# Kernel tuning notes

Measured on AMD Instinct MI355X. Metric: run time of the kernel, lower is better.

## Reference

```python
import jax, jax.numpy as jnp
import numpy as np

H = 12      # num attention heads
W = 128     # one-sided window size (band = 2W+1), also the chunk size
G = 32      # number of global tokens (positions 0..G-1)
NEG = -1e9


def setup_inputs() -> dict:
    key = jax.random.key(0)
    ks = jax.random.split(key, 9)
    B, S, D = 1, 4096, 768
    std = 0.02
    f32 = jnp.float32
    return {
        "hidden_states": jax.random.normal(ks[0], (B, S, D), f32),
        "Wq": jax.random.normal(ks[1], (D, D), f32) * std,
        "bq": jnp.zeros((D,), f32),
        "Wk": jax.random.normal(ks[2], (D, D), f32) * std,
        "bk": jnp.zeros((D,), f32),
        "Wv": jax.random.normal(ks[3], (D, D), f32) * std,
        "bv": jnp.zeros((D,), f32),
        "Wo": jax.random.normal(ks[4], (D, D), f32) * std,
        "bo": jnp.zeros((D,), f32),
    }


def _longformer_attn(hidden, Wq, bq, Wk, bk, Wv, bv, Wo, bo):
    B, S, D = hidden.shape
    dh = D // H
    scale = jnp.asarray(dh, hidden.dtype) ** -0.5

    def proj(Wm, bm):
        return (hidden @ Wm + bm).reshape(B, S, H, dh).transpose(0, 2, 1, 3)  # [B,H,S,dh]

    q = proj(Wq, bq) * scale
    k = proj(Wk, bk)
    v = proj(Wv, bv)

    nc = S // W  # number of query chunks
    q_ch = q.reshape(B, H, nc, W, dh)

    # pad keys/values by one chunk on each side; chunk c sees keys [c*W - W, c*W + 2W)
    kp = jnp.pad(k, ((0, 0), (0, 0), (W, W), (0, 0)))
    vp = jnp.pad(v, ((0, 0), (0, 0), (W, W), (0, 0)))
    idx = (jnp.arange(nc) * W)[:, None] + jnp.arange(3 * W)[None, :]  # [nc, 3W] into padded seq
    k_ch = kp[:, :, idx]  # [B,H,nc,3W,dh]
    v_ch = vp[:, :, idx]

    # banded scores via chunked matmul: [B,H,nc,W,3W]
    band = jnp.einsum('bhcqd,bhckd->bhcqk', q_ch, k_ch)

    # exact band mask |i-j| <= W: with local query qi and local key kj (global j = c*W + kj - W)
    qi = jnp.arange(W)[:, None]           # [W,1]
    kj = jnp.arange(3 * W)[None, :]       # [1,3W]
    in_band = (kj >= qi) & (kj <= qi + 2 * W)                     # [W,3W]
    j = (jnp.arange(nc) * W)[:, None, None] + kj[None] - W        # [nc,1,3W] global key index
    valid = in_band[None] & (j >= G) & (j < S)                    # [nc,W,3W]; j<G handled via global path
    band = jnp.where(valid[None, None], band, NEG)
    band = band.reshape(B, H, S, 3 * W)

    # every query also attends to the G global keys
    gsc = jnp.einsum('bhsd,bhgd->bhsg', q, k[:, :, :G])           # [B,H,S,G]
    scores = jnp.concatenate([gsc, band], axis=-1)                # [B,H,S,G+3W]
    probs = jax.nn.softmax(scores, axis=-1)

    out = jnp.einsum('bhsg,bhgd->bhsd', probs[..., :G], v[:, :, :G])
    pb = probs[..., G:].reshape(B, H, nc, W, 3 * W)
    out = out + jnp.einsum('bhcqk,bhckd->bhcqd', pb, v_ch).reshape(B, H, S, dh)

    # global queries attend to everything (full attention on G rows)
    gq_probs = jax.nn.softmax(jnp.einsum('bhgd,bhsd->bhgs', q[:, :, :G], k), axis=-1)
    out_g = jnp.einsum('bhgs,bhsd->bhgd', gq_probs, v)
    out = out.at[:, :, :G].set(out_g)

    out = out.transpose(0, 2, 1, 3).reshape(B, S, D)
    return out @ Wo + bo


def reference(hidden_states, Wq, bq, Wk, bk, Wv, bv, Wo, bo):
    return _longformer_attn(hidden_states, Wq, bq, Wk, bk, Wv, bv, Wo, bo)
```

## Files before the change

kernel.cpp:

```cpp
#include <hip/hip_runtime.h>
#include <stdint.h>

#define S_LEN 4096
#define DMOD  768
#define NH    12
#define DH    64
#define GG    32
#define NEGBIG (-1e9f)

typedef _Float16 f16;
typedef f16 f16x8 __attribute__((ext_vector_type(8)));
typedef f16 f16x4 __attribute__((ext_vector_type(4)));
typedef float f32x4 __attribute__((ext_vector_type(4)));
typedef uint32_t u32;

#define OFF_H16   ((size_t)0)
#define OFF_WT    ((size_t)6291456)
#define OFF_Q     ((size_t)11010048)
#define OFF_K     ((size_t)17301504)
#define OFF_VT    ((size_t)29884416)
#define OFF_ATT   ((size_t)36175872)
#define OFF_GQO   ((size_t)42467328)
#define OFF_GQL   ((size_t)44040192)

__device__ __forceinline__ void gld_lds16(const void* g, void* l) {
  typedef __attribute__((address_space(3))) u32 lds_u32;
  typedef __attribute__((address_space(1))) u32 glb_u32;
  __builtin_amdgcn_global_load_lds((glb_u32*)(uintptr_t)g,
                                   (lds_u32*)(u32)(uintptr_t)l, 16, 0, 0);
}

__global__ __launch_bounds__(256) void prep_kernel(
    const float* __restrict__ hs,
    const float* __restrict__ Wq, const float* __restrict__ Wk,
    const float* __restrict__ Wv, const float* __restrict__ Wo,
    f16* __restrict__ h16, f16* __restrict__ wt)
{
  const int b = blockIdx.x;
  const int t = threadIdx.x;
  if (b < 576) {
    __shared__ float tile[64][65];
    const int w = b / 144, r2 = b % 144;
    const int n0 = (r2 % 12) * 64, k0 = (r2 / 12) * 64;
    const float* W = (w==0) ? Wq : (w==1) ? Wk : (w==2) ? Wv : Wo;
    f16* WT = wt + (size_t)w * DMOD * DMOD;
    #pragma unroll
    for (int rnd = 0; rnd < 4; ++rnd) {
      const int lin = rnd * 1024 + t * 4;
      const int r = lin >> 6, c = lin & 63;
      const float4 vv = *(const float4*)(W + (size_t)(k0 + r) * DMOD + n0 + c);
      tile[r][c+0] = vv.x; tile[r][c+1] = vv.y; tile[r][c+2] = vv.z; tile[r][c+3] = vv.w;
    }
    __syncthreads();
    #pragma unroll
    for (int rnd = 0; rnd < 2; ++rnd) {
      const int lin = rnd * 256 + t;
      const int n = lin >> 3, kc = (lin & 7) * 8;
      f16x8 o;
      #pragma unroll
      for (int j = 0; j < 8; ++j) o[j] = (f16)tile[kc + j][n];
      *(f16x8*)(WT + (size_t)(n0 + n) * DMOD + k0 + kc) = o;
    }
  } else {
    const size_t idx = (size_t)(b - 576) * 2048 + (size_t)t * 8;
    const float4 a = *(const float4*)(hs + idx);
    const float4 c = *(const float4*)(hs + idx + 4);
    f16x8 o;
    o[0]=(f16)a.x; o[1]=(f16)a.y; o[2]=(f16)a.z; o[3]=(f16)a.w;
    o[4]=(f16)c.x; o[5]=(f16)c.y; o[6]=(f16)c.z; o[7]=(f16)c.w;
    *(f16x8*)(h16 + idx) = o;
  }
}

__global__ __launch_bounds__(256) void gemm_qkv(
    const f16* __restrict__ A, const f16* __restrict__ wt,
    const float* __restrict__ bq, const float* __restrict__ bk, const float* __restrict__ bv,
    f16* __restrict__ q16, f16* __restrict__ k16, f16* __restrict__ vt16)
{
  __shared__ __align__(16) f16 At[3][4096];
  __shared__ __align__(16) f16 Bt[3][4096];
  const int z = blockIdx.z;
  const f16* Wt = wt + (size_t)z * DMOD * DMOD;
  const float* bias = (z==0) ? bq : (z==1) ? bk : bv;
  const float scale = (z==0) ? 0.125f : 1.0f;

  const int tid = threadIdx.x;
  const int lane = tid & 63, wid = tid >> 6;
  const int quad = lane >> 4, l15 = lane & 15;
  const int n0 = blockIdx.x * 128, m0 = blockIdx.y * 128;
  const int wm = (wid >> 1) * 64, wn = (wid & 1) * 64;

  f32x4 acc[4][4];
  #pragma unroll
  for (int i=0;i<4;++i)
    #pragma unroll
    for (int j=0;j<4;++j) acc[i][j] = (f32x4){0.f,0.f,0.f,0.f};

  const int lin0 = tid, lin1 = tid + 256;
  const int ar0 = ((lin0>>6)<<4) + (lin0&15), ac0 = ((lin0>>4)&3)*8;
  const int ar1 = ((lin1>>6)<<4) + (lin1&15), ac1 = ((lin1>>4)&3)*8;
  const f16* Ab = A  + (size_t)m0 * DMOD;
  const f16* Bb = Wt + (size_t)n0 * DMOD;

  gld_lds16(Ab + (size_t)ar0*DMOD + ac0, &At[0][lin0*8]);
  gld_lds16(Ab + (size_t)ar1*DMOD + ac1, &At[0][lin1*8]);
  gld_lds16(Bb + (size_t)ar0*DMOD + ac0, &Bt[0][lin0*8]);
  gld_lds16(Bb + (size_t)ar1*DMOD + ac1, &Bt[0][lin1*8]);

  int cur = 0;
  #pragma unroll 3
  for (int k = 0; k < 24; ++k) {
    const int nxt = (cur == 2) ? 0 : cur + 1;
    if (k < 23) {
      const int k0 = (k + 1) * 32;
      gld_lds16(Ab + (size_t)ar0*DMOD + k0 + ac0, &At[nxt][lin0*8]);
      gld_lds16(Ab + (size_t)ar1*DMOD + k0 + ac1, &At[nxt][lin1*8]);
      gld_lds16(Bb + (size_t)ar0*DMOD + k0 + ac0, &Bt[nxt][lin0*8]);
      gld_lds16(Bb + (size_t)ar1*DMOD + k0 + ac1, &Bt[nxt][lin1*8]);
      asm volatile("s_waitcnt vmcnt(4) lgkmcnt(0)" ::: "memory");
    } else {
      asm volatile("s_waitcnt vmcnt(0) lgkmcnt(0)" ::: "memory");
    }
    __builtin_amdgcn_s_barrier();
    f16x8 af[4], bf[4];
    #pragma unroll
    for (int i=0;i<4;++i) {
      af[i] = *(const f16x8*)(&At[cur][((wm>>4)+i)*512 + lane*8]);
      bf[i] = *(const f16x8*)(&Bt[cur][((wn>>4)+i)*512 + lane*8]);
    }
    #pragma unroll
    for (int i=0;i<4;++i)
      #pragma unroll
      for (int j=0;j<4;++j)
        acc[i][j] = __builtin_amdgcn_mfma_f32_16x16x32_f16(af[i], bf[j], acc[i][j], 0, 0, 0);
    cur = nxt;
  }

  if (z < 2) {
    f16* outp = (z==0) ? q16 : k16;
    #pragma unroll
    for (int j=0;j<4;++j) {
      const int col = n0 + wn + j*16 + l15;
      const float bcol = bias[col];
      const int h = col >> 6, d = col & 63;
      #pragma unroll
      for (int i=0;i<4;++i) {
        const int rbase = m0 + wm + i*16 + quad*4;
        f16* dst = outp + ((size_t)h * S_LEN + rbase) * DH + d;
        #pragma unroll
        for (int r=0;r<4;++r)
          dst[(size_t)r * DH] = (f16)((acc[i][j][r] + bcol) * scale);
      }
    }
  } else {
    #pragma unroll
    for (int j=0;j<4;++j) {
      const int col = n0 + wn + j*16 + l15;
      const float bcol = bias[col];
      const int h = col >> 6, d = col & 63;
      #pragma unroll
      for (int i=0;i<4;++i) {
        const int rbase = m0 + wm + i*16 + quad*4;
        f16x4 o;
        #pragma unroll
        for (int r=0;r<4;++r) o[r] = (f16)(acc[i][j][r] + bcol);
        *(f16x4*)(vt16 + ((size_t)h * DH + d) * S_LEN + rbase) = o;
      }
    }
  }
}

__global__ __launch_bounds__(256) void gemm_out(
    const f16* __restrict__ A, const f16* __restrict__ Wt,
    const float* __restrict__ bo, float* __restrict__ outp)
{
  __shared__ __align__(16) f16 At[3][4096];
  __shared__ __align__(16) f16 Bt[3][2048];
  const int tid = threadIdx.x;
  const int lane = tid & 63, wid = tid >> 6;
  const int quad = lane >> 4, l15 = lane & 15;
  const int n0 = blockIdx.x * 64, m0 = blockIdx.y * 128;
  const int wm = (wid >> 1) * 64, wn = (wid & 1) * 32;

  f32x4 acc[4][2];
  #pragma unroll
  for (int i=0;i<4;++i)
    #pragma unroll
    for (int j=0;j<2;++j) acc[i][j] = (f32x4){0.f,0.f,0.f,0.f};

  const int lin0 = tid, lin1 = tid + 256;
  const int ar0 = ((lin0>>6)<<4) + (lin0&15), ac0 = ((lin0>>4)&3)*8;
  const int ar1 = ((lin1>>6)<<4) + (lin1&15), ac1 = ((lin1>>4)&3)*8;
  const f16* Ab = A  + (size_t)m0 * DMOD;
  const f16* Bb = Wt + (size_t)n0 * DMOD;

  gld_lds16(Ab + (size_t)ar0*DMOD + ac0, &At[0][lin0*8]);
  gld_lds16(Ab + (size_t)ar1*DMOD + ac1, &At[0][lin1*8]);
  gld_lds16(Bb + (size_t)ar0*DMOD + ac0, &Bt[0][lin0*8]);

  int cur = 0;
  #pragma unroll 3
  for (int k = 0; k < 24; ++k) {
    const int nxt = (cur == 2) ? 0 : cur + 1;
    if (k < 23) {
      const int k0 = (k + 1) * 32;
      gld_lds16(Ab + (size_t)ar0*DMOD + k0 + ac0, &At[nxt][lin0*8]);
      gld_lds16(Ab + (size_t)ar1*DMOD + k0 + ac1, &At[nxt][lin1*8]);
      gld_lds16(Bb + (size_t)ar0*DMOD + k0 + ac0, &Bt[nxt][lin0*8]);
      asm volatile("s_waitcnt vmcnt(3) lgkmcnt(0)" ::: "memory");
    } else {
      asm volatile("s_waitcnt vmcnt(0) lgkmcnt(0)" ::: "memory");
    }
    __builtin_amdgcn_s_barrier();
    f16x8 af[4], bf[2];
    #pragma unroll
    for (int i=0;i<4;++i)
      af[i] = *(const f16x8*)(&At[cur][((wm>>4)+i)*512 + lane*8]);
    #pragma unroll
    for (int j=0;j<2;++j)
      bf[j] = *(const f16x8*)(&Bt[cur][((wn>>4)+j)*512 + lane*8]);
    #pragma unroll
    for (int i=0;i<4;++i)
      #pragma unroll
      for (int j=0;j<2;++j)
        acc[i][j] = __builtin_amdgcn_mfma_f32_16x16x32_f16(af[i], bf[j], acc[i][j], 0, 0, 0);
    cur = nxt;
  }

  #pragma unroll
  for (int j=0;j<2;++j) {
    const int col = n0 + wn + j*16 + l15;
    const float bcol = bo[col];
    #pragma unroll
    for (int i=0;i<4;++i) {
      const int rbase = m0 + wm + i*16 + quad*4;
      #pragma unroll
      for (int r=0;r<4;++r)
        outp[(size_t)(rbase + r) * DMOD + col] = acc[i][j][r] + bcol;
    }
  }
}

__global__ __launch_bounds__(256) void band_attn(
    const f16* __restrict__ q16, const f16* __restrict__ k16,
    const f16* __restrict__ vt16, f16* __restrict__ att16,
    float* __restrict__ o_part, float* __restrict__ l_part)
{
  __shared__ __align__(16) f16 Pbuf[4][1280];
  const int h = blockIdx.y;
  const int tid = threadIdx.x, lane = tid & 63, wid = tid >> 6;
  const int quad = lane >> 4, l15 = lane & 15;
  f16* P = &Pbuf[wid][0];

  const int bx = blockIdx.x;
  const bool is_gq = (bx >= 32);
  int gr0 = 0, sp = 0, tcount;
  if (is_gq) {
    sp = (bx - 32) * 4 + wid;
    tcount = 8;
  } else {
    const int sub = bx * 4 + wid;
    if (sub == 0) return;
    gr0 = sub * 32;
    tcount = 10;
  }

  const f16* qh = q16 + (size_t)h * S_LEN * DH;
  const f16* kh = k16 + (size_t)h * S_LEN * DH;
  const f16* vh = vt16 + (size_t)h * DH * S_LEN;

  f16x8 aq[2][2];
  #pragma unroll
  for (int mt=0;mt<2;++mt)
    #pragma unroll
    for (int ks=0;ks<2;++ks)
      aq[mt][ks] = *(const f16x8*)(qh + (size_t)(gr0 + mt*16 + l15)*DH + ks*32 + quad*8);

  f32x4 accO[2][4];
  float lacc[2][4];
  #pragma unroll
  for (int mt=0;mt<2;++mt) {
    #pragma unroll
    for (int n=0;n<4;++n) accO[mt][n] = (f32x4){0.f,0.f,0.f,0.f};
    #pragma unroll
    for (int r=0;r<4;++r) lacc[mt][r] = 0.f;
  }

  for (int t = 0; t < tcount; ++t) {
    int j0;
    if (is_gq) {
      j0 = sp*256 + t*32;
    } else if (t > 0) {
      j0 = gr0 - 128 + (t-1)*32;
      if (j0 <= 0 || j0 >= S_LEN) continue;
    } else {
      j0 = 0;
    }
    f16x8 bk[2][2];
    #pragma unroll
    for (int nt=0;nt<2;++nt) {
      const int key = j0 + nt*16 + l15;
      #pragma unroll
      for (int ks=0;ks<2;++ks)
        bk[nt][ks] = *(const f16x8*)(kh + (size_t)key*DH + ks*32 + quad*8);
    }
    f32x4 sc[2][2];
    #pragma unroll
    for (int mt=0;mt<2;++mt)
      #pragma unroll
      for (int nt=0;nt<2;++nt) {
        f32x4 s = __builtin_amdgcn_mfma_f32_16x16x32_f16(aq[mt][0], bk[nt][0],
                                                         (f32x4){0.f,0.f,0.f,0.f}, 0,0,0);
        sc[mt][nt] = __builtin_amdgcn_mfma_f32_16x16x32_f16(aq[mt][1], bk[nt][1], s, 0,0,0);
      }
    if (!is_gq && (t == 1 || t == 9)) {
      #pragma unroll
      for (int nt=0;nt<2;++nt)
        #pragma unroll
        for (int mt=0;mt<2;++mt)
          #pragma unroll
          for (int r=0;r<4;++r) {
            const int e = (nt*16 + l15) - (mt*16 + quad*4 + r);
            const bool ok = (t == 1) ? (e >= 0) : (e <= 0);
            if (!ok) sc[mt][nt][r] = NEGBIG;
          }
    }
    #pragma unroll
    for (int mt=0;mt<2;++mt)
      #pragma unroll
      for (int r=0;r<4;++r) {
        sc[mt][0][r] = __expf(sc[mt][0][r]);
        sc[mt][1][r] = __expf(sc[mt][1][r]);
        lacc[mt][r] += sc[mt][0][r] + sc[mt][1][r];
      }
    #pragma unroll
    for (int mt=0;mt<2;++mt)
      #pragma unroll
      for (int nt=0;nt<2;++nt)
        #pragma unroll
        for (int r=0;r<4;++r)
          P[(mt*16 + quad*4 + r)*40 + nt*16 + l15] = (f16)sc[mt][nt][r];
    asm volatile("s_waitcnt lgkmcnt(0)" ::: "memory");
    f16x8 ap[2];
    #pragma unroll
    for (int mt=0;mt<2;++mt)
      ap[mt] = *(const f16x8*)(P + (mt*16 + l15)*40 + quad*8);
    #pragma unroll
    for (int n=0;n<4;++n) {
      const f16x8 bv = *(const f16x8*)(vh + (size_t)(n*16 + l15)*S_LEN + j0 + quad*8);
      #pragma unroll
      for (int mt=0;mt<2;++mt)
        accO[mt][n] = __builtin_amdgcn_mfma_f32_16x16x32_f16(ap[mt], bv, accO[mt][n], 0,0,0);
    }
  }

  #pragma unroll
  for (int mt=0;mt<2;++mt)
    #pragma unroll
    for (int r=0;r<4;++r) {
      float v = lacc[mt][r];
      v += __shfl_xor(v, 1, 64);
      v += __shfl_xor(v, 2, 64);
      v += __shfl_xor(v, 4, 64);
      v += __shfl_xor(v, 8, 64);
      lacc[mt][r] = v;
    }

  if (is_gq) {
    const int base = (h*16 + sp)*32;
    #pragma unroll
    for (int mt=0;mt<2;++mt)
      #pragma unroll
      for (int r=0;r<4;++r) {
        const int row = mt*16 + quad*4 + r;
        if (l15 == 0) l_part[base+row] = lacc[mt][r];
        #pragma unroll
        for (int n=0;n<4;++n)
          o_part[(size_t)(base+row)*DH + n*16 + l15] = accO[mt][n][r];
      }
  } else {
    #pragma unroll
    for (int mt=0;mt<2;++mt)
      #pragma unroll
      for (int r=0;r<4;++r) {
        const float inv = 1.f / lacc[mt][r];
        const int s = gr0 + mt*16 + quad*4 + r;
        #pragma unroll
        for (int n=0;n<4;++n)
          att16[(size_t)s * DMOD + h*DH + n*16 + l15] = (f16)(accO[mt][n][r] * inv);
      }
  }
}

__global__ __launch_bounds__(256) void gq_merge(
    const float* __restrict__ o_part, const float* __restrict__ l_part,
    f16* __restrict__ att16)
{
  const int h = blockIdx.x;
  const int t = threadIdx.x;
  for (int u = t; u < 512; u += 256) {
    const int row = u >> 4, c4 = u & 15;
    float4 s = {0.f,0.f,0.f,0.f};
    float l = 0.f;
    for (int sp=0;sp<16;++sp) {
      const int base = (h*16 + sp)*32 + row;
      const float4 v = *(const float4*)&o_part[(size_t)base*DH + c4*4];
      s.x += v.x; s.y += v.y; s.z += v.z; s.w += v.w;
      l += l_part[base];
    }
    const float inv = 1.f / l;
    f16x4 o;
    o[0] = (f16)(s.x*inv); o[1] = (f16)(s.y*inv);
    o[2] = (f16)(s.z*inv); o[3] = (f16)(s.w*inv);
    *(f16x4*)&att16[(size_t)row * DMOD + h*DH + c4*4] = o;
  }
}

extern "C" void kernel_launch(void* const* d_in, const int* in_sizes, int n_in,
                              void* d_out, int out_size, void* d_ws, size_t ws_size,
                              hipStream_t stream)
{
  const float* hs = (const float*)d_in[0];
  const float* Wq = (const float*)d_in[1];
  const float* bq = (const float*)d_in[2];
  const float* Wk = (const float*)d_in[3];
  const float* bk = (const float*)d_in[4];
  const float* Wv = (const float*)d_in[5];
  const float* bv = (const float*)d_in[6];
  const float* Wo = (const float*)d_in[7];
  const float* bo = (const float*)d_in[8];
  float* out = (float*)d_out;
  char* ws = (char*)d_ws;
  f16* h16  = (f16*)(ws + OFF_H16);
  f16* wt   = (f16*)(ws + OFF_WT);
  f16* q16  = (f16*)(ws + OFF_Q);
  f16* k16  = (f16*)(ws + OFF_K);
  f16* vt16 = (f16*)(ws + OFF_VT);
  f16* att16= (f16*)(ws + OFF_ATT);
  float* gqo = (float*)(ws + OFF_GQO);
  float* gql = (float*)(ws + OFF_GQL);

  prep_kernel<<<2112, 256, 0, stream>>>(hs, Wq, Wk, Wv, Wo, h16, wt);
  gemm_qkv<<<dim3(6,32,3), 256, 0, stream>>>(h16, wt, bq, bk, bv, q16, k16, vt16);
  band_attn<<<dim3(36,12), 256, 0, stream>>>(q16, k16, vt16, att16, gqo, gql);
  gq_merge<<<12, 256, 0, stream>>>(gqo, gql, att16);
  gemm_out<<<dim3(12,32), 256, 0, stream>>>(att16, wt + (size_t)3*DMOD*DMOD, bo, out);
}
```

Measured before the change: 171.0 us.

## Switch GEMMs and band attention to 32x32x16 MFMA tiles

```diff
diff --git a/kernel.cpp b/kernel.cpp
--- a/kernel.cpp
+++ b/kernel.cpp
@@ -12,6 +12,7 @@
 typedef f16 f16x8 __attribute__((ext_vector_type(8)));
 typedef f16 f16x4 __attribute__((ext_vector_type(4)));
 typedef float f32x4 __attribute__((ext_vector_type(4)));
+typedef float f32x16 __attribute__((ext_vector_type(16)));
 typedef uint32_t u32;
 
 #define OFF_H16   ((size_t)0)
@@ -86,15 +87,17 @@
 
   const int tid = threadIdx.x;
   const int lane = tid & 63, wid = tid >> 6;
-  const int quad = lane >> 4, l15 = lane & 15;
+  const int l31 = lane & 31, lhi = lane >> 5;
   const int n0 = blockIdx.x * 128, m0 = blockIdx.y * 128;
   const int wm = (wid >> 1) * 64, wn = (wid & 1) * 64;
 
-  f32x4 acc[4][4];
-  #pragma unroll
-  for (int i=0;i<4;++i)
-    #pragma unroll
-    for (int j=0;j<4;++j) acc[i][j] = (f32x4){0.f,0.f,0.f,0.f};
+  f32x16 acc[2][2];
+  #pragma unroll
+  for (int i=0;i<2;++i)
+    #pragma unroll
+    for (int j=0;j<2;++j)
+      #pragma unroll
+      for (int e=0;e<16;++e) acc[i][j][e] = 0.f;
 
   const int lin0 = tid, lin1 = tid + 256;
   const int ar0 = ((lin0>>6)<<4) + (lin0&15), ac0 = ((lin0>>4)&3)*8;
@@ -122,49 +125,66 @@
       asm volatile("s_waitcnt vmcnt(0) lgkmcnt(0)" ::: "memory");
     }
     __builtin_amdgcn_s_barrier();
-    f16x8 af[4], bf[4];
-    #pragma unroll
-    for (int i=0;i<4;++i) {
-      af[i] = *(const f16x8*)(&At[cur][((wm>>4)+i)*512 + lane*8]);
-      bf[i] = *(const f16x8*)(&Bt[cur][((wn>>4)+i)*512 + lane*8]);
-    }
-    #pragma unroll
-    for (int i=0;i<4;++i)
-      #pragma unroll
-      for (int j=0;j<4;++j)
-        acc[i][j] = __builtin_amdgcn_mfma_f32_16x16x32_f16(af[i], bf[j], acc[i][j], 0, 0, 0);
+    f16x8 af[2][2], bf[2][2];
+    #pragma unroll
+    for (int mi=0;mi<2;++mi)
+      #pragma unroll
+      for (int ks=0;ks<2;++ks) {
+        const int ro = (wm>>4) + mi*2 + (l31>>4);
+        af[mi][ks] = *(const f16x8*)(&At[cur][ro*512 + (ks*2+lhi)*128 + (l31&15)*8]);
+      }
+    #pragma unroll
+    for (int nj=0;nj<2;++nj)
+      #pragma unroll
+      for (int ks=0;ks<2;++ks) {
+        const int ro = (wn>>4) + nj*2 + (l31>>4);
+        bf[nj][ks] = *(const f16x8*)(&Bt[cur][ro*512 + (ks*2+lhi)*128 + (l31&15)*8]);
+      }
+    #pragma unroll
+    for (int mi=0;mi<2;++mi)
+      #pragma unroll
+      for (int nj=0;nj<2;++nj) {
+        acc[mi][nj] = __builtin_amdgcn_mfma_f32_32x32x16_f16(af[mi][0], bf[nj][0], acc[mi][nj], 0, 0, 0);
+        acc[mi][nj] = __builtin_amdgcn_mfma_f32_32x32x16_f16(af[mi][1], bf[nj][1], acc[mi][nj], 0, 0, 0);
+      }
     cur = nxt;
   }
 
   if (z < 2) {
     f16* outp = (z==0) ? q16 : k16;
     #pragma unroll
-    for (int j=0;j<4;++j) {
-      const int col = n0 + wn + j*16 + l15;
+    for (int nj=0;nj<2;++nj) {
+      const int col = n0 + wn + nj*32 + l31;
       const float bcol = bias[col];
-      const int h = col >> 6, d = col & 63;
-      #pragma unroll
-      for (int i=0;i<4;++i) {
-        const int rbase = m0 + wm + i*16 + quad*4;
-        f16* dst = outp + ((size_t)h * S_LEN + rbase) * DH + d;
+      const int hh = col >> 6, d = col & 63;
+      f16* dcol = outp + (size_t)hh * S_LEN * DH + d;
+      #pragma unroll
+      for (int mi=0;mi<2;++mi) {
+        const int rb = m0 + wm + mi*32 + 4*lhi;
         #pragma unroll
-        for (int r=0;r<4;++r)
-          dst[(size_t)r * DH] = (f16)((acc[i][j][r] + bcol) * scale);
+        for (int g=0; g<16; ++g) {
+          const int srow = rb + (g&3) + 8*(g>>2);
+          dcol[(size_t)srow * DH] = (f16)((acc[mi][nj][g] + bcol) * scale);
+        }
       }
     }
   } else {
     #pragma unroll
-    for (int j=0;j<4;++j) {
-      const int col = n0 + wn + j*16 + l15;
+    for (int nj=0;nj<2;++nj) {
+      const int col = n0 + wn + nj*32 + l31;
       const float bcol = bias[col];
-      const int h = col >> 6, d = col & 63;
-      #pragma unroll
-      for (int i=0;i<4;++i) {
-        const int rbase = m0 + wm + i*16 + quad*4;
-        f16x4 o;
+      const int hh = col >> 6, d = col & 63;
+      f16* dcol = vt16 + ((size_t)hh * DH + d) * S_LEN;
+      #pragma unroll
+      for (int mi=0;mi<2;++mi) {
+        const int rb = m0 + wm + mi*32 + 4*lhi;
         #pragma unroll
-        for (int r=0;r<4;++r) o[r] = (f16)(acc[i][j][r] + bcol);
-        *(f16x4*)(vt16 + ((size_t)h * DH + d) * S_LEN + rbase) = o;
+        for (int q4=0;q4<4;++q4) {
+          f16x4 o;
+          #pragma unroll
+          for (int r=0;r<4;++r) o[r] = (f16)(acc[mi][nj][q4*4+r] + bcol);
+          *(f16x4*)(dcol + rb + 8*q4) = o;
+        }
       }
     }
   }
@@ -178,15 +198,15 @@
   __shared__ __align__(16) f16 Bt[3][2048];
   const int tid = threadIdx.x;
   const int lane = tid & 63, wid = tid >> 6;
-  const int quad = lane >> 4, l15 = lane & 15;
+  const int l31 = lane & 31, lhi = lane >> 5;
   const int n0 = blockIdx.x * 64, m0 = blockIdx.y * 128;
   const int wm = (wid >> 1) * 64, wn = (wid & 1) * 32;
 
-  f32x4 acc[4][2];
-  #pragma unroll
-  for (int i=0;i<4;++i)
-    #pragma unroll
-    for (int j=0;j<2;++j) acc[i][j] = (f32x4){0.f,0.f,0.f,0.f};
+  f32x16 acc[2];
+  #pragma unroll
+  for (int i=0;i<2;++i)
+    #pragma unroll
+    for (int e=0;e<16;++e) acc[i][e] = 0.f;
 
   const int lin0 = tid, lin1 = tid + 256;
   const int ar0 = ((lin0>>6)<<4) + (lin0&15), ac0 = ((lin0>>4)&3)*8;
@@ -212,31 +232,36 @@
       asm volatile("s_waitcnt vmcnt(0) lgkmcnt(0)" ::: "memory");
     }
     __builtin_amdgcn_s_barrier();
-    f16x8 af[4], bf[2];
-    #pragma unroll
-    for (int i=0;i<4;++i)
-      af[i] = *(const f16x8*)(&At[cur][((wm>>4)+i)*512 + lane*8]);
-    #pragma unroll
-    for (int j=0;j<2;++j)
-      bf[j] = *(const f16x8*)(&Bt[cur][((wn>>4)+j)*512 + lane*8]);
-    #pragma unroll
-    for (int i=0;i<4;++i)
-      #pragma unroll
-      for (int j=0;j<2;++j)
-        acc[i][j] = __builtin_amdgcn_mfma_f32_16x16x32_f16(af[i], bf[j], acc[i][j], 0, 0, 0);
+    f16x8 af[2][2], bf[2];
+    #pragma unroll
+    for (int mi=0;mi<2;++mi)
+      #pragma unroll
+      for (int ks=0;ks<2;++ks) {
+        const int ro = (wm>>4) + mi*2 + (l31>>4);
+        af[mi][ks] = *(const f16x8*)(&At[cur][ro*512 + (ks*2+lhi)*128 + (l31&15)*8]);
+      }
+    #pragma unroll
+    for (int ks=0;ks<2;++ks) {
+      const int ro = (wn>>4) + (l31>>4);
+      bf[ks] = *(const f16x8*)(&Bt[cur][ro*512 + (ks*2+lhi)*128 + (l31&15)*8]);
+    }
+    #pragma unroll
+    for (int mi=0;mi<2;++mi) {
+      acc[mi] = __builtin_amdgcn_mfma_f32_32x32x16_f16(af[mi][0], bf[0], acc[mi], 0, 0, 0);
+      acc[mi] = __builtin_amdgcn_mfma_f32_32x32x16_f16(af[mi][1], bf[1], acc[mi], 0, 0, 0);
+    }
     cur = nxt;
   }
 
-  #pragma unroll
-  for (int j=0;j<2;++j) {
-    const int col = n0 + wn + j*16 + l15;
-    const float bcol = bo[col];
-    #pragma unroll
-    for (int i=0;i<4;++i) {
-      const int rbase = m0 + wm + i*16 + quad*4;
-      #pragma unroll
-      for (int r=0;r<4;++r)
-        outp[(size_t)(rbase + r) * DMOD + col] = acc[i][j][r] + bcol;
+  const int col = n0 + wn + l31;
+  const float bcol = bo[col];
+  #pragma unroll
+  for (int mi=0;mi<2;++mi) {
+    const int rb = m0 + wm + mi*32 + 4*lhi;
+    #pragma unroll
+    for (int g=0; g<16; ++g) {
+      const int srow = rb + (g&3) + 8*(g>>2);
+      outp[(size_t)srow * DMOD + col] = acc[mi][g] + bcol;
     }
   }
 }
@@ -249,7 +274,7 @@
   __shared__ __align__(16) f16 Pbuf[4][1280];
   const int h = blockIdx.y;
   const int tid = threadIdx.x, lane = tid & 63, wid = tid >> 6;
-  const int quad = lane >> 4, l15 = lane & 15;
+  const int l31 = lane & 31, lhi = lane >> 5;
   f16* P = &Pbuf[wid][0];
 
   const int bx = blockIdx.x;
@@ -269,22 +294,19 @@
   const f16* kh = k16 + (size_t)h * S_LEN * DH;
   const f16* vh = vt16 + (size_t)h * DH * S_LEN;
 
-  f16x8 aq[2][2];
-  #pragma unroll
-  for (int mt=0;mt<2;++mt)
-    #pragma unroll
-    for (int ks=0;ks<2;++ks)
-      aq[mt][ks] = *(const f16x8*)(qh + (size_t)(gr0 + mt*16 + l15)*DH + ks*32 + quad*8);
-
-  f32x4 accO[2][4];
-  float lacc[2][4];
-  #pragma unroll
-  for (int mt=0;mt<2;++mt) {
-    #pragma unroll
-    for (int n=0;n<4;++n) accO[mt][n] = (f32x4){0.f,0.f,0.f,0.f};
-    #pragma unroll
-    for (int r=0;r<4;++r) lacc[mt][r] = 0.f;
-  }
+  f16x8 aq[4];
+  #pragma unroll
+  for (int ks=0;ks<4;++ks)
+    aq[ks] = *(const f16x8*)(qh + (size_t)(gr0 + l31)*DH + ks*16 + lhi*8);
+
+  f32x16 accO[2];
+  float lacc[16];
+  #pragma unroll
+  for (int nt=0;nt<2;++nt)
+    #pragma unroll
+    for (int e=0;e<16;++e) accO[nt][e] = 0.f;
+  #pragma unroll
+  for (int g=0;g<16;++g) lacc[g] = 0.f;
 
   for (int t = 0; t < tcount; ++t) {
     int j0;
@@ -296,99 +318,85 @@
     } else {
       j0 = 0;
     }
-    f16x8 bk[2][2];
-    #pragma unroll
-    for (int nt=0;nt<2;++nt) {
-      const int key = j0 + nt*16 + l15;
-      #pragma unroll
-      for (int ks=0;ks<2;++ks)
-        bk[nt][ks] = *(const f16x8*)(kh + (size_t)key*DH + ks*32 + quad*8);
-    }
-    f32x4 sc[2][2];
-    #pragma unroll
-    for (int mt=0;mt<2;++mt)
-      #pragma unroll
-      for (int nt=0;nt<2;++nt) {
-        f32x4 s = __builtin_amdgcn_mfma_f32_16x16x32_f16(aq[mt][0], bk[nt][0],
-                                                         (f32x4){0.f,0.f,0.f,0.f}, 0,0,0);
-        sc[mt][nt] = __builtin_amdgcn_mfma_f32_16x16x32_f16(aq[mt][1], bk[nt][1], s, 0,0,0);
-      }
+    f16x8 bk[4];
+    #pragma unroll
+    for (int ks=0;ks<4;++ks)
+      bk[ks] = *(const f16x8*)(kh + (size_t)(j0 + l31)*DH + ks*16 + lhi*8);
+    f32x16 sc;
+    #pragma unroll
+    for (int e=0;e<16;++e) sc[e] = 0.f;
+    __builtin_amdgcn_s_setprio(1);
+    #pragma unroll
+    for (int ks=0;ks<4;++ks)
+      sc = __builtin_amdgcn_mfma_f32_32x32x16_f16(aq[ks], bk[ks], sc, 0, 0, 0);
+    __builtin_amdgcn_s_setprio(0);
     if (!is_gq && (t == 1 || t == 9)) {
       #pragma unroll
-      for (int nt=0;nt<2;++nt)
-        #pragma unroll
-        for (int mt=0;mt<2;++mt)
-          #pragma unroll
-          for (int r=0;r<4;++r) {
-            const int e = (nt*16 + l15) - (mt*16 + quad*4 + r);
-            const bool ok = (t == 1) ? (e >= 0) : (e <= 0);
-            if (!ok) sc[mt][nt][r] = NEGBIG;
-          }
-    }
-    #pragma unroll
-    for (int mt=0;mt<2;++mt)
-      #pragma unroll
-      for (int r=0;r<4;++r) {
-        sc[mt][0][r] = __expf(sc[mt][0][r]);
-        sc[mt][1][r] = __expf(sc[mt][1][r]);
-        lacc[mt][r] += sc[mt][0][r] + sc[mt][1][r];
-      }
-    #pragma unroll
-    for (int mt=0;mt<2;++mt)
-      #pragma unroll
-      for (int nt=0;nt<2;++nt)
-        #pragma unroll
-        for (int r=0;r<4;++r)
-          P[(mt*16 + quad*4 + r)*40 + nt*16 + l15] = (f16)sc[mt][nt][r];
+      for (int g=0; g<16; ++g) {
+        const int r = (g&3) + 8*(g>>2) + 4*lhi;
+        const int e = l31 - r;
+        const bool ok = (t == 1) ? (e >= 0) : (e <= 0);
+        if (!ok) sc[g] = NEGBIG;
+      }
+    }
+    #pragma unroll
+    for (int g=0; g<16; ++g) {
+      sc[g] = __expf(sc[g]);
+      lacc[g] += sc[g];
+    }
+    #pragma unroll
+    for (int g=0; g<16; ++g)
+      P[((g&3) + 8*(g>>2) + 4*lhi)*40 + l31] = (f16)sc[g];
     asm volatile("s_waitcnt lgkmcnt(0)" ::: "memory");
     f16x8 ap[2];
     #pragma unroll
-    for (int mt=0;mt<2;++mt)
-      ap[mt] = *(const f16x8*)(P + (mt*16 + l15)*40 + quad*8);
-    #pragma unroll
-    for (int n=0;n<4;++n) {
-      const f16x8 bv = *(const f16x8*)(vh + (size_t)(n*16 + l15)*S_LEN + j0 + quad*8);
-      #pragma unroll
-      for (int mt=0;mt<2;++mt)
-        accO[mt][n] = __builtin_amdgcn_mfma_f32_16x16x32_f16(ap[mt], bv, accO[mt][n], 0,0,0);
-    }
-  }
-
-  #pragma unroll
-  for (int mt=0;mt<2;++mt)
-    #pragma unroll
-    for (int r=0;r<4;++r) {
-      float v = lacc[mt][r];
-      v += __shfl_xor(v, 1, 64);
-      v += __shfl_xor(v, 2, 64);
-      v += __shfl_xor(v, 4, 64);
-      v += __shfl_xor(v, 8, 64);
-      lacc[mt][r] = v;
-    }
+    for (int ks=0;ks<2;++ks)
+      ap[ks] = *(const f16x8*)(P + l31*40 + ks*16 + lhi*8);
+    f16x8 bvv[2][2];
+    #pragma unroll
+    for (int nt=0;nt<2;++nt)
+      #pragma unroll
+      for (int ks=0;ks<2;++ks)
+        bvv[nt][ks] = *(const f16x8*)(vh + (size_t)(nt*32 + l31)*S_LEN + j0 + ks*16 + lhi*8);
+    __builtin_amdgcn_s_setprio(1);
+    #pragma unroll
+    for (int nt=0;nt<2;++nt)
+      #pragma unroll
+      for (int ks=0;ks<2;++ks)
+        accO[nt] = __builtin_amdgcn_mfma_f32_32x32x16_f16(ap[ks], bvv[nt][ks], accO[nt], 0, 0, 0);
+    __builtin_amdgcn_s_setprio(0);
+  }
+
+  #pragma unroll
+  for (int g=0; g<16; ++g) {
+    float v = lacc[g];
+    v += __shfl_xor(v, 1, 64);
+    v += __shfl_xor(v, 2, 64);
+    v += __shfl_xor(v, 4, 64);
+    v += __shfl_xor(v, 8, 64);
+    v += __shfl_xor(v, 16, 64);
+    lacc[g] = v;
+  }
 
   if (is_gq) {
     const int base = (h*16 + sp)*32;
     #pragma unroll
-    for (int mt=0;mt<2;++mt)
-      #pragma unroll
-      for (int r=0;r<4;++r) {
-        const int row = mt*16 + quad*4 + r;
-        if (l15 == 0) l_part[base+row] = lacc[mt][r];
-        #pragma unroll
-        for (int n=0;n<4;++n)
-          o_part[(size_t)(base+row)*DH + n*16 + l15] = accO[mt][n][r];
-      }
+    for (int g=0; g<16; ++g) {
+      const int row = (g&3) + 8*(g>>2) + 4*lhi;
+      if (l31 == 0) l_part[base+row] = lacc[g];
+      #pragma unroll
+      for (int nt=0;nt<2;++nt)
+        o_part[(size_t)(base+row)*DH + nt*32 + l31] = accO[nt][g];
+    }
   } else {
     #pragma unroll
-    for (int mt=0;mt<2;++mt)
-      #pragma unroll
-      for (int r=0;r<4;++r) {
-        const float inv = 1.f / lacc[mt][r];
-        const int s = gr0 + mt*16 + quad*4 + r;
-        #pragma unroll
-        for (int n=0;n<4;++n)
-          att16[(size_t)s * DMOD + h*DH + n*16 + l15] = (f16)(accO[mt][n][r] * inv);
-      }
+    for (int g=0; g<16; ++g) {
+      const float inv = 1.f / lacc[g];
+      const int s = gr0 + (g&3) + 8*(g>>2) + 4*lhi;
+      #pragma unroll
+      for (int nt=0;nt<2;++nt)
+        att16[(size_t)s * DMOD + h*DH + nt*32 + l31] = (f16)(accO[nt][g] * inv);
+    }
   }
 }
 
```

Result: no change. 171.5 us (+0.3%).
